# Optimization experiments

Hardware: AMD Instinct MI355X
Metric: run time of the kernel (lower is better)

Reference implementation:

```python
import jax, jax.numpy as jnp
import numpy as np

EPS = 1e-7  # K.epsilon()


def setup_inputs() -> dict:
    key = jax.random.key(0)
    k1, k2, k3 = jax.random.split(key, 3)
    B, T, D = 32, 2048, 1024
    one = jax.random.normal(k1, (B, D), dtype=jnp.float32)
    many = jax.random.normal(k2, (B, T, D), dtype=jnp.float32)
    W = jax.random.normal(k3, (D, D), dtype=jnp.float32) * (1.0 / np.sqrt(D))
    return {"one": one, "many": many, "W": W}


def reference(one, many, W):
    # logits = batch_dot(tanh(many @ W), one, axes=[2,1]) -> [B, T]
    proj = jnp.tanh(jnp.einsum('btd,de->bte', many, W))       # [B,T,D]
    logits = jnp.einsum('btd,bd->bt', proj, one)               # [B,T]
    # stable softmax with Keras epsilon in denominator
    ai = jnp.exp(logits - jnp.max(logits, axis=-1, keepdims=True))
    att_weights = ai / (jnp.sum(ai, axis=-1, keepdims=True) + EPS)  # [B,T]
    result = jnp.einsum('btd,bt->bd', many, att_weights)       # [B,D]
    return result, att_weights
```

## Files before the change

kernel.cpp:

```cpp
#include <hip/hip_runtime.h>
#include <hip/hip_bf16.h>

typedef _Float16 half8v __attribute__((ext_vector_type(8)));
typedef float floatx4 __attribute__((ext_vector_type(4)));

#define NB 32
#define NT 2048
#define ND 1024
#define NM (NB * NT)

__device__ __forceinline__ float fast_tanh(float x) {
    x = fminf(9.0f, fmaxf(-9.0f, x));
    float e = __builtin_amdgcn_exp2f(x * 2.8853900817779268f);
    return (e - 1.0f) * __builtin_amdgcn_rcpf(e + 1.0f);
}

__global__ __launch_bounds__(256)
void wt_kernel(const float* __restrict__ W, _Float16* __restrict__ Wt) {
    __shared__ float tile[32][33];
    int tx = threadIdx.x, ty = threadIdx.y;
    int bx = blockIdx.x, by = blockIdx.y;
    #pragma unroll
    for (int i = 0; i < 4; ++i) {
        int y = by * 32 + ty + i * 8;
        tile[ty + i * 8][tx] = W[y * ND + bx * 32 + tx];
    }
    __syncthreads();
    #pragma unroll
    for (int i = 0; i < 4; ++i) {
        int e = bx * 32 + ty + i * 8;
        Wt[e * ND + by * 32 + tx] = (_Float16)tile[tx][ty + i * 8];
    }
}

__global__ __launch_bounds__(256, 2)
void gemm_logits(const float* __restrict__ many, const _Float16* __restrict__ Wt,
                 const float* __restrict__ one, float* __restrict__ logits) {
    __shared__ _Float16 As[128][72];
    __shared__ _Float16 Bs[128][72];

    int bid = blockIdx.x;
    int j = (bid & 7) * 512 + (bid >> 3);
    int mb = j >> 3, nb = j & 7;
    int m0 = mb * 128, n0 = nb * 128;

    int tid = threadIdx.x;
    int lane = tid & 63, w = tid >> 6;
    int wr = w >> 1, wc = w & 1;
    int l15 = lane & 15, l4 = lane >> 4;

    floatx4 acc[4][4] = {};

    for (int kb = 0; kb < 1024; kb += 64) {
        __syncthreads();
        #pragma unroll
        for (int i = 0; i < 8; ++i) {
            int idx = i * 256 + tid;
            int row = idx >> 4, c4 = idx & 15;
            const float4 v = *reinterpret_cast<const float4*>(
                many + ((size_t)(m0 + row) << 10) + kb + c4 * 4);
            union { _Float16 h[4]; uint2 u; } p;
            p.h[0] = (_Float16)v.x; p.h[1] = (_Float16)v.y;
            p.h[2] = (_Float16)v.z; p.h[3] = (_Float16)v.w;
            *reinterpret_cast<uint2*>(&As[row][c4 * 4]) = p.u;
        }
        #pragma unroll
        for (int i = 0; i < 4; ++i) {
            int idx = i * 256 + tid;
            int row = idx >> 3, c8 = idx & 7;
            uint4 v = *reinterpret_cast<const uint4*>(
                Wt + ((size_t)(n0 + row) << 10) + kb + c8 * 8);
            *reinterpret_cast<uint4*>(&Bs[row][c8 * 8]) = v;
        }
        __syncthreads();
        #pragma unroll
        for (int ks = 0; ks < 64; ks += 32) {
            half8v af[4], bf[4];
            #pragma unroll
            for (int mi = 0; mi < 4; ++mi)
                af[mi] = *reinterpret_cast<const half8v*>(&As[wr * 64 + mi * 16 + l15][ks + l4 * 8]);
            #pragma unroll
            for (int ni = 0; ni < 4; ++ni)
                bf[ni] = *reinterpret_cast<const half8v*>(&Bs[wc * 64 + ni * 16 + l15][ks + l4 * 8]);
            #pragma unroll
            for (int mi = 0; mi < 4; ++mi)
                #pragma unroll
                for (int ni = 0; ni < 4; ++ni)
                    acc[mi][ni] = __builtin_amdgcn_mfma_f32_16x16x32_f16(
                        af[mi], bf[ni], acc[mi][ni], 0, 0, 0);
        }
    }

    int bidx = m0 >> 11;
    float onev[4];
    #pragma unroll
    for (int ni = 0; ni < 4; ++ni)
        onev[ni] = one[(bidx << 10) + n0 + wc * 64 + ni * 16 + l15];

    #pragma unroll
    for (int mi = 0; mi < 4; ++mi) {
        float part[4] = {0.f, 0.f, 0.f, 0.f};
        #pragma unroll
        for (int ni = 0; ni < 4; ++ni)
            #pragma unroll
            for (int b = 0; b < 4; ++b)
                part[b] += fast_tanh(acc[mi][ni][b]) * onev[ni];
        #pragma unroll
        for (int off = 1; off < 16; off <<= 1)
            #pragma unroll
            for (int b = 0; b < 4; ++b)
                part[b] += __shfl_xor(part[b], off, 64);
        #pragma unroll
        for (int b = 0; b < 4; ++b)
            if (l15 == mi * 4 + b)
                atomicAdd(&logits[m0 + wr * 64 + mi * 16 + l4 * 4 + b], part[b]);
    }
}

__global__ __launch_bounds__(256)
void softmax_kernel(const float* __restrict__ logits, float* __restrict__ att) {
    int b = blockIdx.x, tid = threadIdx.x;
    const float* lr = logits + (b << 11);
    float lv[8];
    float mx = -1e30f;
    #pragma unroll
    for (int i = 0; i < 8; ++i) { lv[i] = lr[tid + (i << 8)]; mx = fmaxf(mx, lv[i]); }
    #pragma unroll
    for (int off = 1; off < 64; off <<= 1) mx = fmaxf(mx, __shfl_xor(mx, off, 64));
    __shared__ float redm[4];
    __shared__ float reds[4];
    int wv = tid >> 6;
    if ((tid & 63) == 0) redm[wv] = mx;
    __syncthreads();
    mx = fmaxf(fmaxf(redm[0], redm[1]), fmaxf(redm[2], redm[3]));
    float s = 0.f;
    #pragma unroll
    for (int i = 0; i < 8; ++i) { lv[i] = expf(lv[i] - mx); s += lv[i]; }
    #pragma unroll
    for (int off = 1; off < 64; off <<= 1) s += __shfl_xor(s, off, 64);
    if ((tid & 63) == 0) reds[wv] = s;
    __syncthreads();
    s = reds[0] + reds[1] + reds[2] + reds[3];
    float inv = 1.0f / (s + 1e-7f);
    #pragma unroll
    for (int i = 0; i < 8; ++i) att[(b << 11) + tid + (i << 8)] = lv[i] * inv;
}

__global__ __launch_bounds__(256)
void out_kernel(const float* __restrict__ many, const float* __restrict__ att,
                float* __restrict__ out) {
    int b = blockIdx.x >> 4, tch = blockIdx.x & 15;
    int tid = threadIdx.x;
    __shared__ float aw[128];
    if (tid < 128) aw[tid] = att[(b << 11) + tch * 128 + tid];
    __syncthreads();
    const float* mp = many + (((size_t)b * NT + tch * 128) << 10) + tid * 4;
    float ax = 0.f, ay = 0.f, az = 0.f, aww = 0.f;
    for (int t = 0; t < 128; ++t) {
        float wgt = aw[t];
        float4 v = *reinterpret_cast<const float4*>(mp + ((size_t)t << 10));
        ax = fmaf(v.x, wgt, ax); ay = fmaf(v.y, wgt, ay);
        az = fmaf(v.z, wgt, az); aww = fmaf(v.w, wgt, aww);
    }
    float* op = out + (b << 10) + tid * 4;
    atomicAdd(op + 0, ax); atomicAdd(op + 1, ay);
    atomicAdd(op + 2, az); atomicAdd(op + 3, aww);
}

extern "C" void kernel_launch(void* const* d_in, const int* in_sizes, int n_in,
                              void* d_out, int out_size, void* d_ws, size_t ws_size,
                              hipStream_t stream) {
    const float* one  = (const float*)d_in[0];
    const float* many = (const float*)d_in[1];
    const float* W    = (const float*)d_in[2];
    float* out = (float*)d_out;

    _Float16* Wt  = (_Float16*)d_ws;
    float* logits = (float*)((char*)d_ws + (size_t)ND * ND * 2);
    float* att    = out + NB * ND;

    hipMemsetAsync(out, 0, (size_t)NB * ND * sizeof(float), stream);
    hipMemsetAsync(logits, 0, (size_t)NM * sizeof(float), stream);

    wt_kernel<<<dim3(32, 32), dim3(32, 8), 0, stream>>>(W, Wt);
    gemm_logits<<<4096, 256, 0, stream>>>(many, Wt, one, logits);
    softmax_kernel<<<NB, 256, 0, stream>>>(logits, att);
    out_kernel<<<NB * 16, 256, 0, stream>>>(many, att, out);
}
```

Before: 247.6 us.

## Stream GEMM tiles directly to LDS with XOR swizzle, convert A at fragment load

Replaces the register-staged global-to-LDS copy in the logits GEMM with global_load_lds direct transfers for both the fp32 A tile and the fp16 B tile. It uses an XOR swizzle on 16-byte chunks to avoid LDS bank conflicts. A is now kept as fp32 in LDS and converted to fp16 with cvt_pkrtz when fragments are read. This removes VGPR staging and per-element conversion on the store path. In exchange, LDS use doubles for A, each A fragment needs two LDS reads plus conversions, rounding changes from round-to-nearest to round-toward-zero, and the pipeline is still single-buffered with two barriers per k-step.

```diff
diff --git a/kernel.cpp b/kernel.cpp
--- a/kernel.cpp
+++ b/kernel.cpp
@@ -2,12 +2,18 @@
 #include <hip/hip_bf16.h>
 
 typedef _Float16 half8v __attribute__((ext_vector_type(8)));
+typedef __fp16  fp16x2 __attribute__((ext_vector_type(2)));
 typedef float floatx4 __attribute__((ext_vector_type(4)));
 
 #define NB 32
 #define NT 2048
 #define ND 1024
 #define NM (NB * NT)
+
+#define GL16(g, l)                                                             \
+    __builtin_amdgcn_global_load_lds(                                          \
+        (const __attribute__((address_space(1))) void*)(g),                    \
+        (__attribute__((address_space(3))) void*)(l), 16, 0, 0)
 
 __device__ __forceinline__ float fast_tanh(float x) {
     x = fminf(9.0f, fmaxf(-9.0f, x));
@@ -36,8 +42,10 @@
 __global__ __launch_bounds__(256, 2)
 void gemm_logits(const float* __restrict__ many, const _Float16* __restrict__ Wt,
                  const float* __restrict__ one, float* __restrict__ logits) {
-    __shared__ _Float16 As[128][72];
-    __shared__ _Float16 Bs[128][72];
+    __shared__ uint4 AsQ[2048];
+    __shared__ uint4 BsQ[1024];
+    char* AsB = (char*)AsQ;
+    char* BsB = (char*)BsQ;
 
     int bid = blockIdx.x;
     int j = (bid & 7) * 512 + (bid >> 3);
@@ -49,39 +57,51 @@
     int wr = w >> 1, wc = w & 1;
     int l15 = lane & 15, l4 = lane >> 4;
 
+    const char* aS = (const char*)many
+        + ((size_t)(m0 + (tid >> 4)) << 12)
+        + (size_t)(((tid & 15) ^ ((tid >> 4) & 7)) << 4);
+    const char* bS = (const char*)Wt
+        + ((size_t)(n0 + (tid >> 3)) << 11)
+        + (size_t)(((tid & 7) ^ ((tid >> 3) & 7)) << 4);
+    char* aD = AsB + tid * 16;
+    char* bD = BsB + tid * 16;
+
     floatx4 acc[4][4] = {};
 
     for (int kb = 0; kb < 1024; kb += 64) {
+        #pragma unroll
+        for (int i = 0; i < 8; ++i)
+            GL16(aS + kb * 4 + i * 65536, aD + i * 4096);
+        #pragma unroll
+        for (int i = 0; i < 4; ++i)
+            GL16(bS + kb * 2 + i * 65536, bD + i * 4096);
         __syncthreads();
-        #pragma unroll
-        for (int i = 0; i < 8; ++i) {
-            int idx = i * 256 + tid;
-            int row = idx >> 4, c4 = idx & 15;
-            const float4 v = *reinterpret_cast<const float4*>(
-                many + ((size_t)(m0 + row) << 10) + kb + c4 * 4);
-            union { _Float16 h[4]; uint2 u; } p;
-            p.h[0] = (_Float16)v.x; p.h[1] = (_Float16)v.y;
-            p.h[2] = (_Float16)v.z; p.h[3] = (_Float16)v.w;
-            *reinterpret_cast<uint2*>(&As[row][c4 * 4]) = p.u;
-        }
-        #pragma unroll
-        for (int i = 0; i < 4; ++i) {
-            int idx = i * 256 + tid;
-            int row = idx >> 3, c8 = idx & 7;
-            uint4 v = *reinterpret_cast<const uint4*>(
-                Wt + ((size_t)(n0 + row) << 10) + kb + c8 * 8);
-            *reinterpret_cast<uint4*>(&Bs[row][c8 * 8]) = v;
-        }
-        __syncthreads();
+
         #pragma unroll
         for (int ks = 0; ks < 64; ks += 32) {
             half8v af[4], bf[4];
             #pragma unroll
-            for (int mi = 0; mi < 4; ++mi)
-                af[mi] = *reinterpret_cast<const half8v*>(&As[wr * 64 + mi * 16 + l15][ks + l4 * 8]);
-            #pragma unroll
-            for (int ni = 0; ni < 4; ++ni)
-                bf[ni] = *reinterpret_cast<const half8v*>(&Bs[wc * 64 + ni * 16 + l15][ks + l4 * 8]);
+            for (int mi = 0; mi < 4; ++mi) {
+                int r = wr * 64 + mi * 16 + l15;
+                int s = l15 & 7;
+                const char* base = AsB + r * 256;
+                int c0 = (ks >> 2) + l4 * 2;
+                float4 x = *(const float4*)(base + (size_t)((c0 ^ s) << 4));
+                float4 y = *(const float4*)(base + (size_t)(((c0 + 1) ^ s) << 4));
+                union { fp16x2 p[4]; half8v h; } u;
+                u.p[0] = __builtin_amdgcn_cvt_pkrtz(x.x, x.y);
+                u.p[1] = __builtin_amdgcn_cvt_pkrtz(x.z, x.w);
+                u.p[2] = __builtin_amdgcn_cvt_pkrtz(y.x, y.y);
+                u.p[3] = __builtin_amdgcn_cvt_pkrtz(y.z, y.w);
+                af[mi] = u.h;
+            }
+            #pragma unroll
+            for (int ni = 0; ni < 4; ++ni) {
+                int r = wc * 64 + ni * 16 + l15;
+                int s = l15 & 7;
+                int c = (ks >> 3) + l4;
+                bf[ni] = *(const half8v*)(BsB + r * 128 + (size_t)((c ^ s) << 4));
+            }
             #pragma unroll
             for (int mi = 0; mi < 4; ++mi)
                 #pragma unroll
@@ -89,6 +109,7 @@
                     acc[mi][ni] = __builtin_amdgcn_mfma_f32_16x16x32_f16(
                         af[mi], bf[ni], acc[mi][ni], 0, 0, 0);
         }
+        __syncthreads();
     }
 
     int bidx = m0 >> 11;
@@ -179,8 +200,8 @@
     float* logits = (float*)((char*)d_ws + (size_t)ND * ND * 2);
     float* att    = out + NB * ND;
 
-    hipMemsetAsync(out, 0, (size_t)NB * ND * sizeof(float), stream);
-    hipMemsetAsync(logits, 0, (size_t)NM * sizeof(float), stream);
+    (void)hipMemsetAsync(out, 0, (size_t)NB * ND * sizeof(float), stream);
+    (void)hipMemsetAsync(logits, 0, (size_t)NM * sizeof(float), stream);
 
     wt_kernel<<<dim3(32, 32), dim3(32, 8), 0, stream>>>(W, Wt);
     gemm_logits<<<4096, 256, 0, stream>>>(many, Wt, one, logits);
```

Measured after the change: 242.9 us. Within noise of the previous version (-1.9%).
